# Kernel tuning notes

Measured on AMD Instinct MI355X. Metric: run time of the kernel, lower is better.

Reference implementation:

```python
import jax, jax.numpy as jnp
import numpy as np

# --- static config (matches init_kwargs) ---
B, S, DIM = 1, 2048, 1024
H, G, DK, DV = 16, 4, 64, 64
HPG = H // G
L, D, LSEL, NSEL, W = 32, 16, 64, 16, 512
NCMP = (S - L) // D + 1            # number of compressed blocks over full prefill
J = S // LSEL                      # number of selection blocks
GH = 32                            # gate hidden
NEG = -1e30


def rope(x, pos):
    # x: [B, S, N, Dh]; llama-style half rotation
    Dh = x.shape[-1]
    inv = 1.0 / (10000.0 ** (np.arange(0, Dh, 2) / Dh))
    ang = pos[:, None] * inv[None, :]                      # [S, Dh/2]
    cos = jnp.asarray(np.cos(ang), jnp.float32)[None, :, None, :]
    sin = jnp.asarray(np.sin(ang), jnp.float32)[None, :, None, :]
    x1, x2 = jnp.split(x, 2, axis=-1)
    return jnp.concatenate([x1 * cos - x2 * sin, x2 * cos + x1 * sin], axis=-1)


def masked_softmax(s, m):
    p = jax.nn.softmax(jnp.where(m, s, NEG), axis=-1)
    # rows with no visible keys produce 0 output (empty attention)
    return jnp.where(jnp.any(m, axis=-1, keepdims=True), p, 0.0)


def setup_inputs() -> dict:
    key = jax.random.key(0)
    ks = jax.random.split(key, 12)
    def w(k, shape, fan):
        return jax.random.normal(k, shape, jnp.float32) / np.sqrt(fan)
    return {
        'x': jax.random.normal(ks[0], (B, S, DIM), jnp.float32),
        'W_Q': w(ks[1], (DIM, H * DK), DIM),
        'W_K_sel': w(ks[2], (DIM, G * DK), DIM),
        'W_V_sel': w(ks[3], (DIM, G * DV), DIM),
        'W_K_win': w(ks[4], (DIM, G * DK), DIM),
        'W_V_win': w(ks[5], (DIM, G * DV), DIM),
        'W_K_cmp': w(ks[6], (DIM, G * DK), DIM),
        'W_V_cmp': w(ks[7], (DIM, G * DV), DIM),
        'W_out': w(ks[8], (H * DV, DIM), H * DV),
        'gate_w1': w(ks[9], (DK, GH), DK),
        'gate_b1': jnp.zeros((GH,), jnp.float32),
        'gate_w2': 0.1 * jax.random.normal(ks[10], (GH, 3), jnp.float32),
        'gate_b2': jnp.zeros((3,), jnp.float32),
    }


def reference(x, W_Q, W_K_sel, W_V_sel, W_K_win, W_V_win, W_K_cmp, W_V_cmp,
              W_out, gate_w1, gate_b1, gate_w2, gate_b2):
    pos = np.arange(S)
    s_ = np.arange(S)
    scale = 1.0 / np.sqrt(DK)

    Q = rope((x @ W_Q).reshape(B, S, H, DK), pos).reshape(B, S, G, HPG, DK)

    def proj_kv(Wk, Wv):
        K = rope((x @ Wk).reshape(B, S, G, DK), pos).transpose(0, 2, 1, 3)  # [B,G,S,Dk]
        V = (x @ Wv).reshape(B, S, G, DV).transpose(0, 2, 1, 3)            # [B,G,S,Dv]
        return K, V

    K_sel, V_sel = proj_kv(W_K_sel, W_V_sel)
    K_win, V_win = proj_kv(W_K_win, W_V_win)
    K_cr, V_cr = proj_kv(W_K_cmp, W_V_cmp)

    # --- compressed branch: avg-pool (len L, stride D) of roped K / raw V ---
    bidx = np.arange(NCMP)[:, None] * D + np.arange(L)[None, :]   # [NCMP, L]
    K_cmp = K_cr[:, :, bidx].mean(axis=3)                         # [B,G,NCMP,Dk]
    V_cmp = V_cr[:, :, bidx].mean(axis=3)
    vis_c = (np.arange(NCMP)[None, :] * D + L) <= (s_[:, None] + 1)  # block fully in past
    sc_c = jnp.einsum('bsghd,bgcd->bsghc', Q, K_cmp) * scale
    p_cmp = masked_softmax(sc_c, jnp.asarray(vis_c)[None, :, None, None, :])
    O_cmp = jnp.einsum('bsghc,bgce->bsghe', p_cmp, V_cmp)

    # --- map compressed probs -> selection-block scores (overlap fractions) ---
    i0 = np.arange(NCMP)[:, None] * D
    j0 = np.arange(J)[None, :] * LSEL
    ov = np.maximum(0, np.minimum(i0 + L, j0 + LSEL) - np.maximum(i0, j0)) / L
    p_grp = jnp.einsum('bsghc,cj->bsgj', p_cmp, jnp.asarray(ov, np.float32))  # sum over heads in group

    vis_j = (np.arange(J)[None, :] * LSEL) <= s_[:, None]
    forced = (np.arange(J)[None, :] == 0) | (np.arange(J)[None, :] == (s_ // LSEL)[:, None])
    score = jnp.where(jnp.asarray(vis_j)[None, :, None, :], p_grp, NEG)
    score = jnp.where(jnp.asarray(forced)[None, :, None, :], 1e9, score)  # force block 0 + current block
    topj = jax.lax.top_k(score, NSEL)[1]                                   # [B,S,G,NSEL]
    blk = jax.nn.one_hot(topj, J, dtype=jnp.float32).sum(axis=-2) > 0      # [B,S,G,J]

    tok2blk = np.repeat(np.arange(J), LSEL)[:S]
    causal = s_[:, None] >= s_[None, :]                                    # u <= t
    sel_mask = blk[:, :, :, tok2blk] & jnp.asarray(causal)[None, :, None, :]  # [B,S,G,S]
    sc_s = jnp.einsum('bsghd,bgud->bsghu', Q, K_sel) * scale
    O_sel = jnp.einsum('bsghu,bgue->bsghe',
                       masked_softmax(sc_s, sel_mask[:, :, :, None, :]), V_sel)

    # --- sliding window branch ---
    win_mask = causal & (s_[None, :] > s_[:, None] - W)
    sc_w = jnp.einsum('bsghd,bgud->bsghu', Q, K_win) * scale
    O_win = jnp.einsum('bsghu,bgue->bsghe',
                       masked_softmax(sc_w, jnp.asarray(win_mask)[None, :, None, None, :]), V_win)

    # --- gating MLP on head-pooled query per group ---
    gl = jax.nn.silu(Q.mean(axis=3) @ gate_w1 + gate_b1) @ gate_w2 + gate_b2  # [B,S,G,3]
    pg = jax.nn.softmax(gl, axis=-1)
    t2 = jax.lax.top_k(gl, 2)[0]
    peaked = (t2[..., 0] - t2[..., 1]) > 50.0
    gates = jnp.where(peaked[..., None],
                      jax.nn.one_hot(jnp.argmax(gl, axis=-1), 3, dtype=gl.dtype), pg)

    O = (gates[..., 0, None, None] * O_cmp
         + gates[..., 1, None, None] * O_sel
         + gates[..., 2, None, None] * O_win)          # [B,S,G,h,Dv]
    return O.reshape(B, S, H * DV) @ W_out
```

## Files before the change

### kernel.cpp

```cpp
#include <hip/hip_runtime.h>
#include <math.h>

#define S 2048
#define DIM 1024
#define H 16
#define G 4
#define HPG 4
#define DK 64
#define DV 64
#define NCMP 127
#define JBLK 32
#define NSEL 16
#define WWIN 512
#define GH 32
#define SCL2 0.18033688011112042f

typedef __attribute__((ext_vector_type(8))) __bf16 bf16x8;
typedef __attribute__((ext_vector_type(4))) float f32x4;

__device__ __forceinline__ unsigned short f2bf(float f) {
  unsigned u = __float_as_uint(f);
  unsigned r = (u + 0x7FFFu + ((u >> 16) & 1u)) >> 16;
  return (unsigned short)r;
}

__device__ __forceinline__ unsigned short f2bf_hw(float f) {
  __bf16 b = (__bf16)f;
  return *(unsigned short*)&b;
}

__device__ __forceinline__ float bf2f(unsigned short u) {
  return __uint_as_float((unsigned)u << 16);
}

__device__ __forceinline__ f32x4 mfma16(bf16x8 a, bf16x8 b, f32x4 c) {
  return __builtin_amdgcn_mfma_f32_16x16x32_bf16(a, b, c, 0, 0, 0);
}

__global__ __launch_bounds__(256) void prep(
    const float* __restrict__ x, const float* __restrict__ W0,
    const float* __restrict__ W1, const float* __restrict__ W2,
    const float* __restrict__ W3, const float* __restrict__ W4,
    const float* __restrict__ W_out, float* __restrict__ cosT,
    float* __restrict__ sinT, unsigned short* __restrict__ xb,
    unsigned short* __restrict__ Wt, unsigned short* __restrict__ WtO) {
  __shared__ float t[64 * 65];
  int bid = blockIdx.x, tid = threadIdx.x;
  if (bid < 256) {
    int idx = bid * 256 + tid;
    int s = idx >> 5, i = idx & 31;
    double inv = pow(10000.0, -2.0 * (double)i / 64.0);
    double ang = (double)s * inv;
    cosT[idx] = (float)cos(ang);
    sinT[idx] = (float)sin(ang);
  } else if (bid < 1280) {
    int idx = ((bid - 256) * 256 + tid) * 8;
    float4 a = *(const float4*)&x[idx];
    float4 b = *(const float4*)&x[idx + 4];
    union { unsigned short us[8]; float4 f4; } u;
    u.us[0] = f2bf(a.x); u.us[1] = f2bf(a.y); u.us[2] = f2bf(a.z); u.us[3] = f2bf(a.w);
    u.us[4] = f2bf(b.x); u.us[5] = f2bf(b.y); u.us[6] = f2bf(b.z); u.us[7] = f2bf(b.w);
    *(float4*)&xb[idx] = u.f4;
  } else if (bid < 1600) {
    int p = bid - 1280;
    int m = p / 64;
    int rem = p % 64;
    int k0 = (rem & 15) * 64;
    int n0 = (rem >> 4) * 64;
    const float* W = (m == 0) ? W0 : (m == 1) ? W1 : (m == 2) ? W2 : (m == 3) ? W3 : W4;
    int rr = tid >> 4, c4 = (tid & 15) * 4;
#pragma unroll
    for (int e = 0; e < 4; ++e) {
      int row = rr + e * 16;
      float4 v = *(const float4*)(W + (size_t)(k0 + row) * 256 + n0 + c4);
      t[(c4 + 0) * 65 + row] = v.x;
      t[(c4 + 1) * 65 + row] = v.y;
      t[(c4 + 2) * 65 + row] = v.z;
      t[(c4 + 3) * 65 + row] = v.w;
    }
    __syncthreads();
#pragma unroll
    for (int e = 0; e < 2; ++e) {
      int flat = tid + e * 256;
      int col = flat >> 3, kc = (flat & 7) * 8;
      union { unsigned short us[8]; float4 f4; } u;
#pragma unroll
      for (int i = 0; i < 8; ++i) u.us[i] = f2bf(t[col * 65 + kc + i]);
      *(float4*)(Wt + ((size_t)m * 256 + n0 + col) * 1024 + k0 + kc) = u.f4;
    }
  } else {
    int p = bid - 1600;
    int k0 = (p & 15) * 64;
    int n0 = (p >> 4) * 64;
    int rr = tid >> 4, c4 = (tid & 15) * 4;
#pragma unroll
    for (int e = 0; e < 4; ++e) {
      int row = rr + e * 16;
      float4 v = *(const float4*)(W_out + (size_t)(k0 + row) * 1024 + n0 + c4);
      t[(c4 + 0) * 65 + row] = v.x;
      t[(c4 + 1) * 65 + row] = v.y;
      t[(c4 + 2) * 65 + row] = v.z;
      t[(c4 + 3) * 65 + row] = v.w;
    }
    __syncthreads();
#pragma unroll
    for (int e = 0; e < 2; ++e) {
      int flat = tid + e * 256;
      int col = flat >> 3, kc = (flat & 7) * 8;
      union { unsigned short us[8]; float4 f4; } u;
#pragma unroll
      for (int i = 0; i < 8; ++i) u.us[i] = f2bf(t[col * 65 + kc + i]);
      *(float4*)(WtO + (size_t)(n0 + col) * 1024 + k0 + kc) = u.f4;
    }
  }
}

__device__ __forceinline__ void gemm_body_k(const float* __restrict__ A,
                                            const float* __restrict__ B,
                                            float* __restrict__ C,
                                            int N, int K, int bm, int bn,
                                            int kS, int kE,
                                            float* As , float* Bs ) {
  int tid = threadIdx.x;
  int tr = tid >> 4, tc = tid & 15;
  float acc[4][4] = {{0.f}};
  int arow = tid >> 2;
  int kba = (tid & 3) << 3;
  int brow = tid >> 4;
  int bcol = (tid & 15) << 2;
  const float* Ab = A + (size_t)(bm * 64) * K;
  const float* Bb = B + bn * 64;

  float4 a0 = *(const float4*)(Ab + (size_t)arow * K + kS + kba);
  float4 a1 = *(const float4*)(Ab + (size_t)arow * K + kS + kba + 4);
  float4 b0 = *(const float4*)(Bb + (size_t)(kS + brow) * N + bcol);
  float4 b1 = *(const float4*)(Bb + (size_t)(kS + brow + 16) * N + bcol);

  for (int k0 = kS; k0 < kE; k0 += 32) {
    __syncthreads();
    {
      float av[8] = {a0.x, a0.y, a0.z, a0.w, a1.x, a1.y, a1.z, a1.w};
#pragma unroll
      for (int i = 0; i < 8; ++i) {
        int k = kba + i;
        As[k * 64 + (arow ^ (((k >> 3) & 3) << 3))] = av[i];
      }
      *(float4*)&Bs[brow * 64 + bcol] = b0;
      *(float4*)&Bs[(brow + 16) * 64 + bcol] = b1;
    }
    __syncthreads();
    if (k0 + 32 < kE) {
      a0 = *(const float4*)(Ab + (size_t)arow * K + k0 + 32 + kba);
      a1 = *(const float4*)(Ab + (size_t)arow * K + k0 + 32 + kba + 4);
      b0 = *(const float4*)(Bb + (size_t)(k0 + 32 + brow) * N + bcol);
      b1 = *(const float4*)(Bb + (size_t)(k0 + 32 + brow + 16) * N + bcol);
    }
#pragma unroll
    for (int kk = 0; kk < 32; ++kk) {
      float4 a = *(const float4*)&As[kk * 64 + ((tr << 2) ^ (((kk >> 3) & 3) << 3))];
      float4 b = *(const float4*)&Bs[kk * 64 + (tc << 2)];
      acc[0][0] += a.x * b.x; acc[0][1] += a.x * b.y; acc[0][2] += a.x * b.z; acc[0][3] += a.x * b.w;
      acc[1][0] += a.y * b.x; acc[1][1] += a.y * b.y; acc[1][2] += a.y * b.z; acc[1][3] += a.y * b.w;
      acc[2][0] += a.z * b.x; acc[2][1] += a.z * b.y; acc[2][2] += a.z * b.z; acc[2][3] += a.z * b.w;
      acc[3][0] += a.w * b.x; acc[3][1] += a.w * b.y; acc[3][2] += a.w * b.z; acc[3][3] += a.w * b.w;
    }
  }
  for (int i = 0; i < 4; ++i)
    for (int jj = 0; jj < 4; ++jj)
      C[(size_t)(bm * 64 + (tr << 2) + i) * N + bn * 64 + (tc << 2) + jj] = acc[i][jj];
}

__device__ __forceinline__ void proj_body(
    const unsigned short* __restrict__ xb, const unsigned short* __restrict__ Wt,
    const float* __restrict__ cosT, const float* __restrict__ sinT,
    unsigned short* __restrict__ Kb_s, unsigned short* __restrict__ Vt_s,
    unsigned short* __restrict__ Kb_w, unsigned short* __restrict__ Vt_w,
    unsigned short* __restrict__ Vt_c,
    int s0, int g, int mat, unsigned short* xs, unsigned short* ws) {
  int tid = threadIdx.x, w = tid >> 6, lane = tid & 63;
  int l15 = lane & 15, lg = lane >> 4;
  int rswz = (l15 & 7) << 3;
  bool isV = (mat == 1) || (mat == 3) || (mat == 4);
  const unsigned short* wt = Wt + ((size_t)mat * 256 + g * 64) * 1024;

  f32x4 acc[4];
#pragma unroll
  for (int nt = 0; nt < 4; ++nt) acc[nt] = (f32x4){0.f, 0.f, 0.f, 0.f};

  for (int k0 = 0; k0 < DIM; k0 += 64) {
#pragma unroll
    for (int e = 0; e < 2; ++e) {
      int flat = tid + e * 256;
      int row = flat >> 3, cc = flat & 7;
      int dsti = row * 64 + ((cc ^ (row & 7)) << 3);
      *(float4*)&xs[dsti] = *(const float4*)(xb + (size_t)(s0 + row) * DIM + k0 + cc * 8);
      *(float4*)&ws[dsti] = *(const float4*)(wt + (size_t)row * DIM + k0 + cc * 8);
    }
    __syncthreads();
    const unsigned short* aP = isV ? ws : xs;
    const unsigned short* bP = isV ? xs : ws;
    int arow = w * 16 + l15;
    bf16x8 af[2];
#pragma unroll
    for (int kc = 0; kc < 2; ++kc)
      af[kc] = *(const bf16x8*)&aP[(arow * 64 + kc * 32 + lg * 8) ^ rswz];
#pragma unroll
    for (int nt = 0; nt < 4; ++nt) {
      int brow = nt * 16 + l15;
      bf16x8 b0 = *(const bf16x8*)&bP[(brow * 64 + lg * 8) ^ rswz];
      bf16x8 b1 = *(const bf16x8*)&bP[(brow * 64 + 32 + lg * 8) ^ rswz];
      acc[nt] = mfma16(af[0], b0, acc[nt]);
      acc[nt] = mfma16(af[1], b1, acc[nt]);
    }
    __syncthreads();
  }

  if (!isV) {
    unsigned short* Kb = (mat == 0) ? Kb_s : Kb_w;
#pragma unroll
    for (int rr = 0; rr < 4; ++rr) {
      int tok = s0 + w * 16 + lg * 4 + rr;
#pragma unroll
      for (int p = 0; p < 2; ++p) {
        int i = p * 16 + l15;
        float c = cosT[tok * 32 + i], sn = sinT[tok * 32 + i];
        float x1 = acc[p][rr], x2 = acc[p + 2][rr];
        Kb[((size_t)g * S + tok) * 64 + i] = f2bf(x1 * c - x2 * sn);
        Kb[((size_t)g * S + tok) * 64 + i + 32] = f2bf(x2 * c + x1 * sn);
      }
    }
  } else {
    unsigned short* Vt = (mat == 1) ? Vt_s : (mat == 3) ? Vt_w : Vt_c;
#pragma unroll
    for (int rr = 0; rr < 4; ++rr) {
      int col = w * 16 + lg * 4 + rr;
#pragma unroll
      for (int nt = 0; nt < 4; ++nt) {
        int tok = s0 + nt * 16 + l15;
        Vt[((size_t)g * 64 + col) * S + tok] = f2bf(acc[nt][rr]);
      }
    }
  }
}

__global__ __launch_bounds__(256) void qk_proj(
    const float* __restrict__ x, const float* __restrict__ W_Q,
    const float* __restrict__ W_Kc, float* __restrict__ Pq, float* __restrict__ Pk,
    const unsigned short* __restrict__ xb, const unsigned short* __restrict__ Wt,
    const float* __restrict__ cosT, const float* __restrict__ sinT,
    unsigned short* __restrict__ Kb_s, unsigned short* __restrict__ Vt_s,
    unsigned short* __restrict__ Kb_w, unsigned short* __restrict__ Vt_w,
    unsigned short* __restrict__ Vt_c) {
  __shared__ __align__(16) float lds_f[4096];
  int bid = blockIdx.x;
  int r = bid % 3;
  if (r < 2) {
    int gid = (bid / 3) * 2 + r;
    int z = gid / 640;
    int rem = gid % 640;
    int ct = rem % 20;
    int bm = rem / 20;
    int kS = z * 512, kE = kS + 512;
    float* As = lds_f;
    float* Bs = lds_f + 2048;
    if (ct < 16)
      gemm_body_k(x, W_Q, Pq + (size_t)z * S * 1024, 1024, DIM, bm, ct, kS, kE, As, Bs);
    else
      gemm_body_k(x, W_Kc, Pk + (size_t)z * S * 256, 256, DIM, bm, ct - 16, kS, kE, As, Bs);
  } else {
    int pid = bid / 3;
    int s0b = pid % 32;
    int g = (pid / 32) % 4;
    int mat = pid / 128;
    unsigned short* xs = (unsigned short*)lds_f;
    unsigned short* ws = xs + 4096;
    proj_body(xb, Wt, cosT, sinT, Kb_s, Vt_s, Kb_w, Vt_w, Vt_c, s0b * 64, g, mat,
              xs, ws);
  }
}

__global__ __launch_bounds__(256) void reduce_rope(
    const float* __restrict__ Pq, const float* __restrict__ Pk,
    const float* __restrict__ cosT, const float* __restrict__ sinT,
    float* __restrict__ Qb, unsigned short* __restrict__ Qbf,
    float* __restrict__ Kcr) {
  int idx = blockIdx.x * 256 + threadIdx.x;
  const int NQ = S * H * 32;
  if (idx < NQ) {
    int i = idx & 31;
    int rest = idx >> 5;
    int h = rest & 15;
    int s = rest >> 4;
    size_t base = (size_t)s * 1024 + h * 64 + i;
    float a1 = Pq[base] + Pq[(size_t)S * 1024 + base];
    float a2 = Pq[base + 32] + Pq[(size_t)S * 1024 + base + 32];
    float c = cosT[s * 32 + i], sn = sinT[s * 32 + i];
    float q1 = a1 * c - a2 * sn, q2 = a2 * c + a1 * sn;
    Qb[base] = q1;
    Qb[base + 32] = q2;
    Qbf[base] = f2bf(q1);
    Qbf[base + 32] = f2bf(q2);
  } else {
    int j = idx - NQ;
    if (j >= S * G * 32) return;
    int i = j & 31;
    int rest = j >> 5;
    int g = rest & 3;
    int s = rest >> 2;
    size_t base = (size_t)s * 256 + g * 64 + i;
    float a1 = Pk[base] + Pk[(size_t)S * 256 + base];
    float a2 = Pk[base + 32] + Pk[(size_t)S * 256 + base + 32];
    float c = cosT[s * 32 + i], sn = sinT[s * 32 + i];
    Kcr[base] = a1 * c - a2 * sn;
    Kcr[base + 32] = a2 * c + a1 * sn;
  }
}

__global__ __launch_bounds__(256) void post_reduce(
    const float* __restrict__ Kcr, const unsigned short* __restrict__ Vtc,
    float* __restrict__ Kc, float* __restrict__ Vc, const float* __restrict__ Q,
    const float* __restrict__ w1, const float* __restrict__ b1,
    const float* __restrict__ w2, const float* __restrict__ b2,
    float* __restrict__ gates) {
  int bid = blockIdx.x, tid = threadIdx.x;
  if (bid < 127) {
    int item = bid * 256 + tid;
    int c = item >> 8;
    int g = (item >> 6) & 3;
    int d = item & 63;
    float sk = 0.f, sv = 0.f;
    const unsigned short* vrow = Vtc + ((size_t)g * 64 + d) * S + c * 16;
    for (int l = 0; l < 32; ++l) {
      sk += Kcr[(size_t)((c * 16 + l) * G + g) * 64 + d];
      sv += bf2f(vrow[l]);
    }
    Kc[(size_t)(g * NCMP + c) * 64 + d] = sk * (1.f / 32.f);
    Vc[(size_t)(g * NCMP + c) * 64 + d] = sv * (1.f / 32.f);
  } else {
    int idx = (bid - 127) * 256 + tid;
    int s = idx >> 2, g = idx & 3;
    float qm[64];
#pragma unroll
    for (int d = 0; d < 64; ++d) {
      float a = 0.f;
      for (int hp = 0; hp < HPG; ++hp) a += Q[(size_t)(s * H + g * HPG + hp) * 64 + d];
      qm[d] = a * 0.25f;
    }
    float gl[3] = {b2[0], b2[1], b2[2]};
    for (int j = 0; j < GH; ++j) {
      float z = b1[j];
      for (int d = 0; d < 64; ++d) z += qm[d] * w1[d * GH + j];
      float sl = z / (1.f + expf(-z));
      gl[0] += sl * w2[j * 3 + 0];
      gl[1] += sl * w2[j * 3 + 1];
      gl[2] += sl * w2[j * 3 + 2];
    }
    float m = fmaxf(gl[0], fmaxf(gl[1], gl[2]));
    float e0 = expf(gl[0] - m), e1 = expf(gl[1] - m), e2 = expf(gl[2] - m);
    float inv = 1.f / (e0 + e1 + e2);
    float p0 = e0 * inv, p1 = e1 * inv, p2 = e2 * inv;
    int am = (gl[0] >= gl[1] && gl[0] >= gl[2]) ? 0 : ((gl[1] >= gl[2]) ? 1 : 2);
    float t1 = (am == 0) ? fmaxf(gl[1], gl[2])
                         : ((am == 1) ? fmaxf(gl[0], gl[2]) : fmaxf(gl[0], gl[1]));
    if (m - t1 > 50.f) {
      p0 = (am == 0) ? 1.f : 0.f;
      p1 = (am == 1) ? 1.f : 0.f;
      p2 = (am == 2) ? 1.f : 0.f;
    }
    gates[idx * 3 + 0] = p0;
    gates[idx * 3 + 1] = p1;
    gates[idx * 3 + 2] = p2;
  }
}

__device__ __forceinline__ void cmp_body(const float* __restrict__ Q,
                                         const float* __restrict__ Kc,
                                         const float* __restrict__ Vc,
                                         float* __restrict__ Ocmp,
                                         unsigned int* __restrict__ selm,
                                         int s, int g,
                                         float* q4, float* sc, float* pg) {
  int tid = threadIdx.x;
  int nvis = (s >= 31) ? (((s - 31) >> 4) + 1) : 0;
  {
    int h = tid >> 6, d = tid & 63;
    q4[h * 64 + d] = Q[(size_t)(s * H + g * HPG + h) * 64 + d];
  }
  __syncthreads();

  if (tid < 128) {
    int c = tid;
    if (c < nvis) {
      float a0 = 0.f, a1 = 0.f, a2 = 0.f, a3 = 0.f;
      const float* kr = &Kc[(size_t)(g * NCMP + c) * 64];
#pragma unroll 4
      for (int kk = 0; kk < 16; ++kk) {
        float4 kv = *(const float4*)&kr[kk * 4];
        float4 q0 = *(const float4*)&q4[0 * 64 + kk * 4];
        float4 q1 = *(const float4*)&q4[1 * 64 + kk * 4];
        float4 q2 = *(const float4*)&q4[2 * 64 + kk * 4];
        float4 q3 = *(const float4*)&q4[3 * 64 + kk * 4];
        a0 += q0.x * kv.x + q0.y * kv.y + q0.z * kv.z + q0.w * kv.w;
        a1 += q1.x * kv.x + q1.y * kv.y + q1.z * kv.z + q1.w * kv.w;
        a2 += q2.x * kv.x + q2.y * kv.y + q2.z * kv.z + q2.w * kv.w;
        a3 += q3.x * kv.x + q3.y * kv.y + q3.z * kv.z + q3.w * kv.w;
      }
      sc[0 * 128 + c] = a0 * 0.125f;
      sc[1 * 128 + c] = a1 * 0.125f;
      sc[2 * 128 + c] = a2 * 0.125f;
      sc[3 * 128 + c] = a3 * 0.125f;
    } else {
      sc[0 * 128 + c] = -INFINITY;
      sc[1 * 128 + c] = -INFINITY;
      sc[2 * 128 + c] = -INFINITY;
      sc[3 * 128 + c] = -INFINITY;
    }
  }
  __syncthreads();

  int w = tid >> 6, lane = tid & 63;
  {
    float v0 = sc[w * 128 + lane];
    float v1 = (lane + 64 < NCMP) ? sc[w * 128 + lane + 64] : -INFINITY;
    float m = fmaxf(v0, v1);
    for (int off = 32; off; off >>= 1) m = fmaxf(m, __shfl_xor(m, off));
    float e0 = (m > -INFINITY && v0 > -INFINITY) ? expf(v0 - m) : 0.f;
    float e1 = (m > -INFINITY && v1 > -INFINITY) ? expf(v1 - m) : 0.f;
    float sum = e0 + e1;
    for (int off = 32; off; off >>= 1) sum += __shfl_xor(sum, off);
    float inv = (sum > 0.f) ? 1.f / sum : 0.f;
    sc[w * 128 + lane] = e0 * inv;
    if (lane + 64 < NCMP) sc[w * 128 + lane + 64] = e1 * inv;
    if (lane == 63) sc[w * 128 + 127] = 0.f;
  }
  __syncthreads();

  {
    int h = tid >> 6, d = tid & 63;
    float o = 0.f;
#pragma unroll 4
    for (int c = 0; c < nvis; ++c)
      o += sc[h * 128 + c] * Vc[(size_t)(g * NCMP + c) * 64 + d];
    Ocmp[(size_t)(s * H + g * HPG + h) * 64 + d] = o;
  }

  if (tid < JBLK) {
    int j = tid;
    float a = 0.f;
#pragma unroll
    for (int h = 0; h < 4; ++h) {
      const float* row = &sc[h * 128];
      float v = row[4 * j] + row[4 * j + 1] + row[4 * j + 2] + 0.5f * row[4 * j + 3];
      if (j > 0) v += 0.5f * row[4 * j - 1];
      a += v;
    }
    pg[j] = a;
  }
  __syncthreads();

  if (tid < 64) {
    int j = tid & 31;
    int cur = s >> 6;
    float v = (j * 64 <= s) ? pg[j] : -1e30f;
    if (j == 0 || j == cur) v = 1e9f;
    unsigned int mask = 0;
#pragma unroll 1
    for (int n = 0; n < NSEL; ++n) {
      float bv = v;
      int bj = j;
#pragma unroll
      for (int off = 1; off < 32; off <<= 1) {
        float ov = __shfl_xor(bv, off);
        int oj = __shfl_xor(bj, off);
        if (ov > bv || (ov == bv && oj < bj)) { bv = ov; bj = oj; }
      }
      mask |= 1u << bj;
      if (j == bj) v = -INFINITY;
    }
    if (tid == 0) selm[(size_t)s * G + g] = mask;
  }
}

__global__ __launch_bounds__(256) void cmp_attn(const float* __restrict__ Qb,
                                                const float* __restrict__ Kc,
                                                const float* __restrict__ Vc,
                                                float* __restrict__ Ocmp,
                                                unsigned int* __restrict__ selm) {
  __shared__ float q4[256];
  __shared__ float sc[512];
  __shared__ float pg[JBLK];
  cmp_body(Qb, Kc, Vc, Ocmp, selm, blockIdx.x, blockIdx.y, q4, sc, pg);
}

template <int MODE>
__device__ __forceinline__ void attn_body(
    const unsigned short* __restrict__ Qbf, const unsigned short* __restrict__ Kb,
    const unsigned short* __restrict__ Vtb, const unsigned int* __restrict__ selm,
    float* __restrict__ O, int t0, int g,
    unsigned short* Kl, unsigned short* Vt, unsigned short* Pl,
    unsigned int* sel_l, int* blist, int* nB_p) {
  int tid = threadIdx.x;
  int w = tid >> 6, lane = tid & 63;
  int l15 = lane & 15, lg = lane >> 4;
  int rswz = (l15 & 7) << 3;
  int jdiag = t0 >> 6;

  if (MODE == 0 && tid < 16) sel_l[tid] = selm[(t0 + tid) * G + g];
  __syncthreads();
  if (tid == 0) {
    int n = 0;
    if (MODE == 0) {
      unsigned int un = 0;
      for (int i = 0; i < 16; ++i) un |= sel_l[i];
      for (int j = 0; j <= jdiag; ++j)
        if ((un >> j) & 1u) blist[n++] = j;
    } else {
      int lo = t0 - (WWIN - 1);
      int j0 = (lo > 0) ? (lo >> 6) : 0;
      for (int j = j0; j <= jdiag; ++j) blist[n++] = j;
    }
    *nB_p = n;
  }
  __syncthreads();
  int nB = *nB_p;

  int tok = t0 + l15;
  bf16x8 qf[2];
  {
    const unsigned short* qb = Qbf + ((size_t)tok * H + g * HPG + w) * 64;
    qf[0] = *(const bf16x8*)(qb + lg * 8);
    qf[1] = *(const bf16x8*)(qb + 32 + lg * 8);
  }

  float mrun = -INFINITY, lrun = 0.f;
  f32x4 oacc[4];
#pragma unroll
  for (int dt = 0; dt < 4; ++dt) oacc[dt] = (f32x4){0.f, 0.f, 0.f, 0.f};

  for (int b = 0; b < nB; ++b) {
    int j = blist[b];
    int ku = j * 64;

    {
      const unsigned short* src = Kb + ((size_t)g * S + ku) * 64;
#pragma unroll
      for (int c2 = 0; c2 < 2; ++c2) {
        int chunk = tid + c2 * 256;
        int key = chunk >> 3, cc = chunk & 7;
        *(float4*)&Kl[key * 64 + ((cc ^ (key & 7)) << 3)] =
            *(const float4*)(src + chunk * 8);
      }
#pragma unroll
      for (int c2 = 0; c2 < 2; ++c2) {
        int chunk = tid + c2 * 256;
        int dim = chunk >> 3, cc = chunk & 7;
        *(float4*)&Vt[dim * 64 + ((cc ^ (dim & 7)) << 3)] =
            *(const float4*)(Vtb + ((size_t)g * 64 + dim) * S + ku + cc * 8);
      }
    }
    __syncthreads();

    f32x4 sf[4];
#pragma unroll
    for (int kt = 0; kt < 4; ++kt) sf[kt] = (f32x4){0.f, 0.f, 0.f, 0.f};
#pragma unroll
    for (int kt = 0; kt < 4; ++kt) {
      int krow = kt * 16 + l15;
      bf16x8 kf0 = *(const bf16x8*)&Kl[(krow * 64 + lg * 8) ^ rswz];
      bf16x8 kf1 = *(const bf16x8*)&Kl[(krow * 64 + 32 + lg * 8) ^ rswz];
      sf[kt] = mfma16(kf0, qf[0], sf[kt]);
      sf[kt] = mfma16(kf1, qf[1], sf[kt]);
    }

    bool bsel = true;
    if (MODE == 0) bsel = ((sel_l[l15] >> j) & 1u) != 0;
    float sv2[4][4];
    if (j == jdiag) {
#pragma unroll
      for (int kt = 0; kt < 4; ++kt)
#pragma unroll
        for (int rr = 0; rr < 4; ++rr) {
          int u = ku + kt * 16 + lg * 4 + rr;
          sv2[kt][rr] = (u <= tok) ? sf[kt][rr] * SCL2 : -INFINITY;
        }
    } else if (MODE == 1 && (ku + WWIN <= t0 + 15)) {
#pragma unroll
      for (int kt = 0; kt < 4; ++kt)
#pragma unroll
        for (int rr = 0; rr < 4; ++rr) {
          int u = ku + kt * 16 + lg * 4 + rr;
          sv2[kt][rr] = (u + WWIN > tok) ? sf[kt][rr] * SCL2 : -INFINITY;
        }
    } else {
#pragma unroll
      for (int kt = 0; kt < 4; ++kt)
#pragma unroll
        for (int rr = 0; rr < 4; ++rr) sv2[kt][rr] = sf[kt][rr] * SCL2;
    }

    float pmax = -INFINITY;
#pragma unroll
    for (int kt = 0; kt < 4; ++kt)
#pragma unroll
      for (int rr = 0; rr < 4; ++rr) pmax = fmaxf(pmax, sv2[kt][rr]);
    pmax = fmaxf(pmax, __shfl_xor(pmax, 16));
    pmax = fmaxf(pmax, __shfl_xor(pmax, 32));
    if (MODE == 0 && !bsel) pmax = -INFINITY;

    if (__any(pmax > mrun)) {
      float mnew = fmaxf(mrun, pmax);
      float mc = (mnew == -INFINITY) ? 0.f : mnew;
      float fac = exp2f(mrun - mc);
      mrun = mnew;
      lrun *= fac;
#pragma unroll
      for (int dt = 0; dt < 4; ++dt)
#pragma unroll
        for (int rr = 0; rr < 4; ++rr) oacc[dt][rr] *= fac;
    }
    float mcb = (MODE == 0 && !bsel) ? INFINITY
                                     : ((mrun == -INFINITY) ? 0.f : mrun);

    float psum = 0.f;
    unsigned short pb[16];
#pragma unroll
    for (int kt = 0; kt < 4; ++kt)
#pragma unroll
      for (int rr = 0; rr < 4; ++rr) {
        float e = exp2f(sv2[kt][rr] - mcb);
        psum += e;
        pb[kt * 4 + rr] = f2bf_hw(e);
      }
    psum += __shfl_xor(psum, 16);
    psum += __shfl_xor(psum, 32);
    lrun += psum;

    {
      unsigned short* pw = Pl + w * 1024;
#pragma unroll
      for (int kt = 0; kt < 4; ++kt) {
        int idx = (l15 * 64 + kt * 16 + lg * 4) ^ rswz;
        unsigned int lo = (unsigned)pb[kt * 4] | ((unsigned)pb[kt * 4 + 1] << 16);
        unsigned int hi = (unsigned)pb[kt * 4 + 2] | ((unsigned)pb[kt * 4 + 3] << 16);
        *(uint2*)&pw[idx] = make_uint2(lo, hi);
      }
    }

#pragma unroll
    for (int kc = 0; kc < 2; ++kc) {
      bf16x8 pf = *(const bf16x8*)&Pl[w * 1024 + ((l15 * 64 + kc * 32 + lg * 8) ^ rswz)];
#pragma unroll
      for (int dt = 0; dt < 4; ++dt) {
        bf16x8 vf = *(const bf16x8*)&Vt[((dt * 16 + l15) * 64 + kc * 32 + lg * 8) ^ rswz];
        oacc[dt] = mfma16(vf, pf, oacc[dt]);
      }
    }
    __syncthreads();
  }

  {
    float inv = (lrun > 0.f) ? 1.f / lrun : 0.f;
    float* ob = O + ((size_t)tok * H + g * HPG + w) * 64;
#pragma unroll
    for (int dt = 0; dt < 4; ++dt) {
      float4 v;
      v.x = oacc[dt][0] * inv;
      v.y = oacc[dt][1] * inv;
      v.z = oacc[dt][2] * inv;
      v.w = oacc[dt][3] * inv;
      *(float4*)(ob + dt * 16 + lg * 4) = v;
    }
  }
}

__global__ __launch_bounds__(256) void attn_fused(
    const unsigned short* __restrict__ Qbf,
    const unsigned short* __restrict__ Kbs, const unsigned short* __restrict__ Vts,
    const unsigned short* __restrict__ Kbw, const unsigned short* __restrict__ Vtw,
    const unsigned int* __restrict__ selm,
    float* __restrict__ Osel, float* __restrict__ Owin) {
  __shared__ unsigned short Kl[4096];
  __shared__ unsigned short Vt[4096];
  __shared__ unsigned short Pl[4096];
  __shared__ unsigned int sel_l[16];
  __shared__ int blist[JBLK];
  __shared__ int nB_s;
  int t0 = blockIdx.x * 16;
  int g = blockIdx.y;
  if (blockIdx.z == 0)
    attn_body<0>(Qbf, Kbs, Vts, selm, Osel, t0, g, Kl, Vt, Pl, sel_l, blist, &nB_s);
  else
    attn_body<1>(Qbf, Kbw, Vtw, nullptr, Owin, t0, g, Kl, Vt, Pl, sel_l, blist,
                 &nB_s);
}

__global__ void combine(const float* __restrict__ Oc, const float* __restrict__ Os,
                        const float* __restrict__ Ow, const float* __restrict__ gates,
                        unsigned short* __restrict__ Ob) {
  int idx = blockIdx.x * blockDim.x + threadIdx.x;
  if (idx >= S * H * DV) return;
  int h = (idx >> 6) & 15;
  int s = idx >> 10;
  int g = h >> 2;
  const float* gp = &gates[(size_t)(s * G + g) * 3];
  Ob[idx] = f2bf(gp[0] * Oc[idx] + gp[1] * Os[idx] + gp[2] * Ow[idx]);
}

__global__ __launch_bounds__(256) void gemm_out(const unsigned short* __restrict__ Ob,
                                                const unsigned short* __restrict__ Wt,
                                                float* __restrict__ out) {
  __shared__ unsigned short xs[64 * 64];
  __shared__ unsigned short ws[64 * 64];
  int s0 = blockIdx.x * 64;
  int n0 = blockIdx.y * 64;
  int tid = threadIdx.x, w = tid >> 6, lane = tid & 63;
  int l15 = lane & 15, lg = lane >> 4;
  int rswz = (l15 & 7) << 3;

  f32x4 acc[4];
#pragma unroll
  for (int nt = 0; nt < 4; ++nt) acc[nt] = (f32x4){0.f, 0.f, 0.f, 0.f};

  for (int k0 = 0; k0 < DIM; k0 += 64) {
#pragma unroll
    for (int e = 0; e < 2; ++e) {
      int flat = tid + e * 256;
      int row = flat >> 3, cc = flat & 7;
      int dsti = row * 64 + ((cc ^ (row & 7)) << 3);
      *(float4*)&xs[dsti] = *(const float4*)(Ob + (size_t)(s0 + row) * DIM + k0 + cc * 8);
      *(float4*)&ws[dsti] = *(const float4*)(Wt + (size_t)(n0 + row) * DIM + k0 + cc * 8);
    }
    __syncthreads();
    int arow = w * 16 + l15;
    bf16x8 af0 = *(const bf16x8*)&xs[(arow * 64 + lg * 8) ^ rswz];
    bf16x8 af1 = *(const bf16x8*)&xs[(arow * 64 + 32 + lg * 8) ^ rswz];
#pragma unroll
    for (int nt = 0; nt < 4; ++nt) {
      int brow = nt * 16 + l15;
      bf16x8 b0 = *(const bf16x8*)&ws[(brow * 64 + lg * 8) ^ rswz];
      bf16x8 b1 = *(const bf16x8*)&ws[(brow * 64 + 32 + lg * 8) ^ rswz];
      acc[nt] = mfma16(af0, b0, acc[nt]);
      acc[nt] = mfma16(af1, b1, acc[nt]);
    }
    __syncthreads();
  }

#pragma unroll
  for (int nt = 0; nt < 4; ++nt)
#pragma unroll
    for (int rr = 0; rr < 4; ++rr)
      out[(size_t)(s0 + w * 16 + lg * 4 + rr) * 1024 + n0 + nt * 16 + l15] =
          acc[nt][rr];
}

extern "C" void kernel_launch(void* const* d_in, const int* in_sizes, int n_in,
                              void* d_out, int out_size, void* d_ws, size_t ws_size,
                              hipStream_t stream) {
  const float* x = (const float*)d_in[0];
  const float* W_Q = (const float*)d_in[1];
  const float* W_K_sel = (const float*)d_in[2];
  const float* W_V_sel = (const float*)d_in[3];
  const float* W_K_win = (const float*)d_in[4];
  const float* W_V_win = (const float*)d_in[5];
  const float* W_K_cmp = (const float*)d_in[6];
  const float* W_V_cmp = (const float*)d_in[7];
  const float* W_out = (const float*)d_in[8];
  const float* gw1 = (const float*)d_in[9];
  const float* gb1 = (const float*)d_in[10];
  const float* gw2 = (const float*)d_in[11];
  const float* gb2 = (const float*)d_in[12];

  float* w = (float*)d_ws;
  float* cosT = w;  w += S * 32;
  float* sinT = w;  w += S * 32;
  float* Qb   = w;  w += S * H * DK;
  float* Kcr  = w;  w += S * G * DK;
  float* Kc   = w;  w += G * NCMP * DK;
  float* Vc   = w;  w += G * NCMP * DV;
  float* Ocmp = w;  w += S * H * DV;
  float* Osel = w;  w += S * H * DV;
  float* Owin = w;  w += S * H * DV;
  float* gates= w;  w += S * G * 3;
  unsigned int* selm = (unsigned int*)w;  w += S * G;
  unsigned short* Kbf_s = (unsigned short*)w;  w += (size_t)G * S * 64 / 2;
  unsigned short* Kbf_w = (unsigned short*)w;  w += (size_t)G * S * 64 / 2;
  unsigned short* Vt_s  = (unsigned short*)w;  w += (size_t)G * S * 64 / 2;
  unsigned short* Vt_w  = (unsigned short*)w;  w += (size_t)G * S * 64 / 2;
  unsigned short* Vt_c  = (unsigned short*)w;  w += (size_t)G * S * 64 / 2;
  unsigned short* Qbf   = (unsigned short*)w;  w += (size_t)S * H * 64 / 2;
  unsigned short* xb    = (unsigned short*)w;  w += (size_t)S * DIM / 2;
  unsigned short* Wt    = (unsigned short*)w;  w += (size_t)5 * 256 * DIM / 2;
  unsigned short* Ob    = (unsigned short*)w;  w += (size_t)S * H * DV / 2;
  unsigned short* WtO   = (unsigned short*)w;  w += (size_t)DIM * DIM / 2;

  float* Pq = Ocmp;
  float* Pk = Owin;

  prep<<<1856, 256, 0, stream>>>(x, W_K_sel, W_V_sel, W_K_win, W_V_win, W_V_cmp,
                                 W_out, cosT, sinT, xb, Wt, WtO);

  qk_proj<<<1920, 256, 0, stream>>>(x, W_Q, W_K_cmp, Pq, Pk, xb, Wt, cosT, sinT,
                                    Kbf_s, Vt_s, Kbf_w, Vt_w, Vt_c);
  reduce_rope<<<(S * (H + G) * 32 + 255) / 256, 256, 0, stream>>>(
      Pq, Pk, cosT, sinT, Qb, Qbf, Kcr);

  post_reduce<<<159, 256, 0, stream>>>(Kcr, Vt_c, Kc, Vc, Qb, gw1, gb1, gw2, gb2,
                                       gates);

  cmp_attn<<<dim3(S, G), 256, 0, stream>>>(Qb, Kc, Vc, Ocmp, selm);
  attn_fused<<<dim3(S / 16, G, 2), 256, 0, stream>>>(Qbf, Kbf_s, Vt_s, Kbf_w, Vt_w,
                                                     selm, Osel, Owin);

  combine<<<(S * H * DV + 255) / 256, 256, 0, stream>>>(Ocmp, Osel, Owin, gates, Ob);

  gemm_out<<<dim3(S / 64, DIM / 64), 256, 0, stream>>>(Ob, WtO, (float*)d_out);
}
```

Measured before the change: 281.7 us.

## Fuse compressed attention with sliding-window attention and alias P buffer onto K

```diff
diff --git a/kernel.cpp b/kernel.cpp
--- a/kernel.cpp
+++ b/kernel.cpp
@@ -481,29 +481,19 @@
   }
 }
 
-__global__ __launch_bounds__(256) void cmp_attn(const float* __restrict__ Qb,
-                                                const float* __restrict__ Kc,
-                                                const float* __restrict__ Vc,
-                                                float* __restrict__ Ocmp,
-                                                unsigned int* __restrict__ selm) {
-  __shared__ float q4[256];
-  __shared__ float sc[512];
-  __shared__ float pg[JBLK];
-  cmp_body(Qb, Kc, Vc, Ocmp, selm, blockIdx.x, blockIdx.y, q4, sc, pg);
-}
-
 template <int MODE>
 __device__ __forceinline__ void attn_body(
     const unsigned short* __restrict__ Qbf, const unsigned short* __restrict__ Kb,
     const unsigned short* __restrict__ Vtb, const unsigned int* __restrict__ selm,
     float* __restrict__ O, int t0, int g,
-    unsigned short* Kl, unsigned short* Vt, unsigned short* Pl,
+    unsigned short* Kl, unsigned short* Vt,
     unsigned int* sel_l, int* blist, int* nB_p) {
   int tid = threadIdx.x;
   int w = tid >> 6, lane = tid & 63;
   int l15 = lane & 15, lg = lane >> 4;
   int rswz = (l15 & 7) << 3;
   int jdiag = t0 >> 6;
+  unsigned short* Pl = Kl;
 
   if (MODE == 0 && tid < 16) sel_l[tid] = selm[(t0 + tid) * G + g];
   __syncthreads();
@@ -571,6 +561,7 @@
       sf[kt] = mfma16(kf0, qf[0], sf[kt]);
       sf[kt] = mfma16(kf1, qf[1], sf[kt]);
     }
+    __syncthreads();
 
     bool bsel = true;
     if (MODE == 0) bsel = ((sel_l[l15] >> j) & 1u) != 0;
@@ -673,25 +664,46 @@
   }
 }
 
-__global__ __launch_bounds__(256) void attn_fused(
-    const unsigned short* __restrict__ Qbf,
-    const unsigned short* __restrict__ Kbs, const unsigned short* __restrict__ Vts,
+__global__ __launch_bounds__(256) void cmp_win(
+    const float* __restrict__ Qb, const float* __restrict__ Kc,
+    const float* __restrict__ Vc, float* __restrict__ Ocmp,
+    unsigned int* __restrict__ selm, const unsigned short* __restrict__ Qbf,
     const unsigned short* __restrict__ Kbw, const unsigned short* __restrict__ Vtw,
-    const unsigned int* __restrict__ selm,
-    float* __restrict__ Osel, float* __restrict__ Owin) {
+    float* __restrict__ Owin) {
+  __shared__ __align__(16) unsigned char ldsb[16768];
+  int bid = blockIdx.x;
+  if (bid % 17 != 16) {
+    int cid = (bid / 17) * 16 + (bid % 17);
+    int s = cid >> 2, g = cid & 3;
+    float* q4 = (float*)ldsb;
+    float* sc = q4 + 256;
+    float* pg = sc + 512;
+    cmp_body(Qb, Kc, Vc, Ocmp, selm, s, g, q4, sc, pg);
+  } else {
+    int pid = bid / 17;
+    int t0 = (pid & 127) * 16;
+    int g = pid >> 7;
+    unsigned short* Kl = (unsigned short*)ldsb;
+    unsigned short* Vt = Kl + 4096;
+    int* blist = (int*)(Vt + 4096);
+    int* nB_p = blist + JBLK;
+    attn_body<1>(Qbf, Kbw, Vtw, nullptr, Owin, t0, g, Kl, Vt, nullptr, blist,
+                 nB_p);
+  }
+}
+
+__global__ __launch_bounds__(256) void attn_sel(
+    const unsigned short* __restrict__ Qbf, const unsigned short* __restrict__ Kbs,
+    const unsigned short* __restrict__ Vts, const unsigned int* __restrict__ selm,
+    float* __restrict__ Osel) {
   __shared__ unsigned short Kl[4096];
   __shared__ unsigned short Vt[4096];
-  __shared__ unsigned short Pl[4096];
   __shared__ unsigned int sel_l[16];
   __shared__ int blist[JBLK];
   __shared__ int nB_s;
   int t0 = blockIdx.x * 16;
   int g = blockIdx.y;
-  if (blockIdx.z == 0)
-    attn_body<0>(Qbf, Kbs, Vts, selm, Osel, t0, g, Kl, Vt, Pl, sel_l, blist, &nB_s);
-  else
-    attn_body<1>(Qbf, Kbw, Vtw, nullptr, Owin, t0, g, Kl, Vt, Pl, sel_l, blist,
-                 &nB_s);
+  attn_body<0>(Qbf, Kbs, Vts, selm, Osel, t0, g, Kl, Vt, sel_l, blist, &nB_s);
 }
 
 __global__ void combine(const float* __restrict__ Oc, const float* __restrict__ Os,
@@ -807,9 +819,8 @@
   post_reduce<<<159, 256, 0, stream>>>(Kcr, Vt_c, Kc, Vc, Qb, gw1, gb1, gw2, gb2,
                                        gates);
 
-  cmp_attn<<<dim3(S, G), 256, 0, stream>>>(Qb, Kc, Vc, Ocmp, selm);
-  attn_fused<<<dim3(S / 16, G, 2), 256, 0, stream>>>(Qbf, Kbf_s, Vt_s, Kbf_w, Vt_w,
-                                                     selm, Osel, Owin);
+  cmp_win<<<8704, 256, 0, stream>>>(Qb, Kc, Vc, Ocmp, selm, Qbf, Kbf_w, Vt_w, Owin);
+  attn_sel<<<dim3(S / 16, G), 256, 0, stream>>>(Qbf, Kbf_s, Vt_s, selm, Osel);
 
   combine<<<(S * H * DV + 255) / 256, 256, 0, stream>>>(Ocmp, Osel, Owin, gates, Ob);
 
```

Measured after the change: 313.7 us. +11.4%, slower.
